# Kernel optimization log

Measured on AMD Instinct MI355X. Metric: run time of the kernel, lower is better.

Reference implementation:

```python
import jax, jax.numpy as jnp
import numpy as np

B, C, H, W = 128, 512, 14, 14
P = 512  # num_parts (codebook size)


def setup_inputs() -> dict:
    key = jax.random.key(0)
    k1, k2, k3 = jax.random.split(key, 3)
    fm = jax.random.normal(k1, (B, C, H, W), dtype=jnp.float32)
    embedding = jax.random.normal(k2, (B, C), dtype=jnp.float32)
    # self.w = torch.randn(P, C).clamp_(min=0)
    w = jnp.maximum(jax.random.normal(k3, (P, C), dtype=jnp.float32), 0.0)
    w_ep_sum = w  # clone of w at init
    w_ep_num = jnp.ones((P,), dtype=jnp.float32)
    return {"fm": fm, "embedding": embedding, "w": w,
            "w_ep_sum": w_ep_sum, "w_ep_num": w_ep_num, "epoch": 5}


def reference(fm, embedding, w, w_ep_sum, w_ep_num, epoch):
    b, c, h, wd = fm.shape
    p = w.shape[0]
    # NCHW -> [B, HW, C]
    x = jnp.transpose(fm, (0, 2, 3, 1)).reshape(b, h * wd, c)
    xf = x.reshape(b * h * wd, c)
    dist = (jnp.sum(xf * xf, axis=1, keepdims=True)
            + jnp.sum(w * w, axis=1)
            - 2.0 * (xf @ w.T))                      # [B*HW, P]
    assign = jax.nn.softmax(-dist.reshape(b, h * wd, p), axis=-1)
    # hard threshold: zero out weak assignments
    assign = jnp.where(assign < 1.0 / p, 0.0, assign)  # [B, HW, P]
    assign_sum = assign.mean(axis=1)                    # [B, P]

    if epoch > 2:  # epoch is a static Python int
        # relu(einsum('bn,nc->bnc').mean(1)) == relu((assign_sum @ w) / P)
        cvec = jax.nn.relu((assign_sum @ w) / p)        # [B, C]
        embedding_cat = jnp.concatenate([embedding, cvec], axis=-1)
    else:
        embedding_cat = jnp.concatenate([embedding, jnp.zeros_like(embedding)], axis=-1)

    # collect_weight (no-grad EMA-style accumulate).
    # einsum('bmn,bmc->bmnc').sum(1).sum(0) == einsum('bmn,bmc->nc') -- avoids
    # materializing the [B,M,N,C] tensor the torch code builds.
    update_w = jnp.einsum('bmn,bmc->nc', assign, x)     # [P, C]
    assign_mean = jnp.sum(assign, axis=(0, 1))          # [P]
    upd = assign_mean > 1.0
    new_w_ep_sum = jnp.where(upd[:, None], w_ep_sum + update_w, w_ep_sum)
    new_w_ep_num = jnp.where(upd, w_ep_num + assign_mean, w_ep_num)
    return embedding_cat, new_w_ep_sum, new_w_ep_num
```

## Files before the change

### kernel.cpp

```cpp
#include <hip/hip_runtime.h>
#include <hip/hip_bf16.h>

#define Bn   128
#define Cn   512
#define HWn  196
#define Mn   25088
#define Pn   512
#define SPLITK2 32
#define KCH  1024

#define OFF_XT     0u
#define OFF_AT     8388608u
#define OFF_PART   16777216u
#define OFF_XM     16777216u
#define OFF_WF     25165824u
#define OFF_WNORM  25296896u
#define OFF_RAWP   25297408u
#define OFF_MEAN   25559552u

#define OUT_CAT  0u
#define OUT_WSUM 131072u
#define OUT_WNUM 393216u

using bf16x8 = __attribute__((ext_vector_type(8))) short;
using f16x8  = __attribute__((ext_vector_type(8))) _Float16;
using f32x4  = __attribute__((ext_vector_type(4))) float;

__device__ __forceinline__ unsigned short f2b(float f) {
    union { float f; unsigned u; } x; x.f = f;
    unsigned r = x.u + 0x7fffu + ((x.u >> 16) & 1u);
    return (unsigned short)(r >> 16);
}

__global__ __launch_bounds__(64) void k_wnorm(const float* __restrict__ w,
                                              float* __restrict__ wn,
                                              _Float16* __restrict__ wf) {
    int n = blockIdx.x, l = threadIdx.x;
    const float* p = w + (size_t)n * Cn + l * 8;
    float4 a = *(const float4*)p;
    float4 b = *(const float4*)(p + 4);
    float s = a.x*a.x + a.y*a.y + a.z*a.z + a.w*a.w
            + b.x*b.x + b.y*b.y + b.z*b.z + b.w*b.w;
    alignas(16) _Float16 h[8];
    h[0]=(_Float16)a.x; h[1]=(_Float16)a.y; h[2]=(_Float16)a.z; h[3]=(_Float16)a.w;
    h[4]=(_Float16)b.x; h[5]=(_Float16)b.y; h[6]=(_Float16)b.z; h[7]=(_Float16)b.w;
    *(float4*)(wf + (size_t)(n >> 4) * 8192u + (size_t)(l >> 2) * 512
                 + (n & 15) * 32 + (l & 3) * 8) = *(const float4*)h;
    #pragma unroll
    for (int o = 32; o > 0; o >>= 1) s += __shfl_down(s, o);
    if (l == 0) wn[n] = s;
}

__global__ __launch_bounds__(512) void k_prep2(const float* __restrict__ fm,
                                               _Float16* __restrict__ xm,
                                               unsigned short* __restrict__ xt) {
    __shared__ _Float16 tile[64][200];
    int b = blockIdx.x;
    int cg = blockIdx.y * 64;
    int t = threadIdx.x;
    for (int i = t; i < 64 * 49; i += 512) {
        int cl = i / 49, h4 = i - cl * 49;
        float4 v = *(const float4*)(fm + ((size_t)(b * Cn + cg + cl) * HWn) + h4 * 4);
        tile[cl][h4*4+0] = (_Float16)v.x;
        tile[cl][h4*4+1] = (_Float16)v.y;
        tile[cl][h4*4+2] = (_Float16)v.z;
        tile[cl][h4*4+3] = (_Float16)v.w;
    }
    __syncthreads();
    for (int i = t; i < HWn * 8; i += 512) {
        int hw = i >> 3, seg = i & 7;
        alignas(16) _Float16 h[8];
        #pragma unroll
        for (int j = 0; j < 8; ++j) h[j] = tile[seg * 8 + j][hw];
        *(float4*)(xm + (size_t)(b * HWn + hw) * Cn + cg + seg * 8) = *(const float4*)h;
    }
    for (int i = t; i < 64 * 4 * 16; i += 512) {
        int cl = i >> 6, rem = i & 63;
        int q = rem >> 4, j4 = rem & 15;
        ushort4 o;
        if (j4 < 12) {
            o.x = f2b((float)tile[cl][q*49 + j4*4 + 0]);
            o.y = f2b((float)tile[cl][q*49 + j4*4 + 1]);
            o.z = f2b((float)tile[cl][q*49 + j4*4 + 2]);
            o.w = f2b((float)tile[cl][q*49 + j4*4 + 3]);
        } else if (j4 == 12) {
            o.x = f2b((float)tile[cl][q*49 + 48]);
            o.y = 0; o.z = 0; o.w = 0;
        } else {
            o.x = 0; o.y = 0; o.z = 0; o.w = 0;
        }
        int c = cg + cl;
        int T = c >> 4;
        int seg = b * 8 + q * 2 + (j4 >> 3);
        int k = (j4 & 7) * 4;
        *(ushort4*)(xt + (size_t)T * 524288u + (size_t)seg * 512 + (c & 15) * 32 + k) = o;
    }
}

__global__ __launch_bounds__(512, 2) void k_post(const _Float16* __restrict__ xm,
                                                 const _Float16* __restrict__ wf,
                                                 const float* __restrict__ wnorm,
                                                 unsigned short* __restrict__ at,
                                                 float* __restrict__ rawp) {
    __shared__ _Float16 As[64][72];
    __shared__ float redmx[64][8];
    __shared__ float redsm[64][8];
    const int bid = blockIdx.x;
    const int b = bid >> 2, q = bid & 3;
    const int tid = threadIdx.x;
    const int nq = tid >> 6, lane = tid & 63;
    const int rl = lane & 15, rq = lane >> 4;
    const int kb = rq * 8;
    const int m0 = b * 196 + q * 49;
    const int n0 = nq * 64;
    const int srow = tid >> 3;
    const int skc  = tid & 7;
    const bool sOK = srow < 49;
    const _Float16* asrc = xm + (size_t)(m0 + srow) * Cn + skc * 8;

    if (!sOK) {
        f16x8 z = {};
        *(f16x8*)&As[srow][skc * 8] = z;
    }
    if (sOK) *(f16x8*)&As[srow][skc * 8] = *(const f16x8*)asrc;
    __syncthreads();

    const _Float16* wtb = wf + (size_t)(nq * 4) * 8192u + rl * 32 + kb;

    f32x4 acc[4][4] = {};
    for (int c = 0; c < 8; ++c) {
        #pragma unroll
        for (int ks = 0; ks < 2; ++ks) {
            const int seg = c * 2 + ks;
            f16x8 a[4], bb[4];
            #pragma unroll
            for (int f = 0; f < 4; ++f)
                a[f] = *(const f16x8*)&As[f * 16 + rl][ks * 32 + kb];
            #pragma unroll
            for (int g = 0; g < 4; ++g)
                bb[g] = *(const f16x8*)(wtb + (size_t)g * 8192u + seg * 512);
            #pragma unroll
            for (int f = 0; f < 4; ++f)
                #pragma unroll
                for (int g = 0; g < 4; ++g)
                    acc[f][g] = __builtin_amdgcn_mfma_f32_16x16x32_f16(a[f], bb[g], acc[f][g], 0, 0, 0);
        }
        if (c < 7) {
            __syncthreads();
            if (sOK)
                *(f16x8*)&As[srow][skc * 8] = *(const f16x8*)(asrc + (c + 1) * 64);
            __syncthreads();
        }
    }
    float wn4[4];
    #pragma unroll
    for (int g = 0; g < 4; ++g) wn4[g] = wnorm[n0 + g * 16 + rl];
    #pragma unroll
    for (int f = 0; f < 4; ++f)
        #pragma unroll
        for (int g = 0; g < 4; ++g)
            #pragma unroll
            for (int r = 0; r < 4; ++r)
                acc[f][g][r] = 2.0f * acc[f][g][r] - wn4[g];
    float mx[4][4];
    #pragma unroll
    for (int f = 0; f < 4; ++f)
        #pragma unroll
        for (int r = 0; r < 4; ++r) {
            float m_ = fmaxf(fmaxf(acc[f][0][r], acc[f][1][r]),
                             fmaxf(acc[f][2][r], acc[f][3][r]));
            #pragma unroll
            for (int o = 8; o >= 1; o >>= 1) m_ = fmaxf(m_, __shfl_xor(m_, o));
            mx[f][r] = m_;
        }
    if (rl == 0)
        #pragma unroll
        for (int f = 0; f < 4; ++f)
            #pragma unroll
            for (int r = 0; r < 4; ++r)
                redmx[f * 16 + rq * 4 + r][nq] = mx[f][r];
    __syncthreads();
    float rmax[4][4];
    #pragma unroll
    for (int f = 0; f < 4; ++f)
        #pragma unroll
        for (int r = 0; r < 4; ++r) {
            const float* p = redmx[f * 16 + rq * 4 + r];
            rmax[f][r] = fmaxf(fmaxf(fmaxf(p[0], p[1]), fmaxf(p[2], p[3])),
                               fmaxf(fmaxf(p[4], p[5]), fmaxf(p[6], p[7])));
        }
    float sm[4][4];
    #pragma unroll
    for (int f = 0; f < 4; ++f)
        #pragma unroll
        for (int r = 0; r < 4; ++r) {
            float s_ = 0.f;
            #pragma unroll
            for (int g = 0; g < 4; ++g) {
                float p = __expf(acc[f][g][r] - rmax[f][r]);
                acc[f][g][r] = p;
                s_ += p;
            }
            #pragma unroll
            for (int o = 8; o >= 1; o >>= 1) s_ += __shfl_xor(s_, o);
            sm[f][r] = s_;
        }
    if (rl == 0)
        #pragma unroll
        for (int f = 0; f < 4; ++f)
            #pragma unroll
            for (int r = 0; r < 4; ++r)
                redsm[f * 16 + rq * 4 + r][nq] = sm[f][r];
    __syncthreads();
    const float invP = 1.0f / 512.0f;
    #pragma unroll
    for (int f = 0; f < 4; ++f)
        #pragma unroll
        for (int r = 0; r < 4; ++r) {
            const float* p = redsm[f * 16 + rq * 4 + r];
            float inv = 1.0f / (p[0] + p[1] + p[2] + p[3] + p[4] + p[5] + p[6] + p[7]);
            #pragma unroll
            for (int g = 0; g < 4; ++g) {
                float a = acc[f][g][r] * inv;
                acc[f][g][r] = (a < invP) ? 0.0f : a;
            }
        }
    float cs[4] = {};
    #pragma unroll
    for (int g = 0; g < 4; ++g) {
        #pragma unroll
        for (int f = 0; f < 4; ++f)
            #pragma unroll
            for (int r = 0; r < 4; ++r)
                if (f * 16 + rq * 4 + r < 49) cs[g] += acc[f][g][r];
        cs[g] += __shfl_xor(cs[g], 16);
        cs[g] += __shfl_xor(cs[g], 32);
    }
    if (rq == 0)
        #pragma unroll
        for (int g = 0; g < 4; ++g)
            rawp[(size_t)bid * 512 + n0 + g * 16 + rl] = cs[g];
    const int segbase = b * 8 + q * 2;
    #pragma unroll
    for (int f = 0; f < 4; ++f) {
        const int mloc = f * 16 + rq * 4;
        const int sa = segbase + (mloc >> 5);
        const int k = mloc & 31;
        #pragma unroll
        for (int g = 0; g < 4; ++g) {
            ushort4 o;
            o.x = (mloc + 0 < 49) ? f2b(acc[f][g][0]) : (unsigned short)0;
            o.y = (mloc + 1 < 49) ? f2b(acc[f][g][1]) : (unsigned short)0;
            o.z = (mloc + 2 < 49) ? f2b(acc[f][g][2]) : (unsigned short)0;
            o.w = (mloc + 3 < 49) ? f2b(acc[f][g][3]) : (unsigned short)0;
            const int T = nq * 4 + g;
            *(ushort4*)(at + (size_t)T * 524288u + (size_t)sa * 512 + rl * 32 + k) = o;
        }
    }
}

__global__ __launch_bounds__(256) void k_reduce(const float* __restrict__ rawp,
                                                const float* __restrict__ wnum,
                                                float* __restrict__ mean,
                                                float* __restrict__ outnum) {
    int n = blockIdx.x * 256 + threadIdx.x;
    float s = 0.f;
    for (int r = 0; r < 512; ++r) s += rawp[(size_t)r * Pn + n];
    mean[n] = s;
    outnum[n] = wnum[n] + (s > 1.0f ? s : 0.0f);
}

__global__ __launch_bounds__(256) void k_cvec(const float* __restrict__ rawp,
                                              const float* __restrict__ w,
                                              const float* __restrict__ emb,
                                              const int* __restrict__ epoch,
                                              float* __restrict__ out) {
    __shared__ float srow[512];
    int b = blockIdx.x, t = threadIdx.x;
    float s0 = 0.f, s1 = 0.f;
    #pragma unroll
    for (int q = 0; q < 4; ++q) {
        s0 += rawp[(size_t)(4 * b + q) * Pn + t];
        s1 += rawp[(size_t)(4 * b + q) * Pn + t + 256];
    }
    srow[t] = s0;
    srow[t + 256] = s1;
    __syncthreads();
    float a0 = 0.f, a1 = 0.f;
    for (int p = 0; p < Pn; ++p) {
        float ap = srow[p];
        a0 = fmaf(ap, w[(size_t)p * Cn + t], a0);
        a1 = fmaf(ap, w[(size_t)p * Cn + t + 256], a1);
    }
    const float sc = 1.0f / (196.0f * 512.0f);
    int ep = epoch[0];
    float c0 = (ep > 2) ? fmaxf(a0, 0.f) * sc : 0.f;
    float c1 = (ep > 2) ? fmaxf(a1, 0.f) * sc : 0.f;
    out[(size_t)b * 1024 + t]             = emb[(size_t)b * Cn + t];
    out[(size_t)b * 1024 + t + 256]       = emb[(size_t)b * Cn + t + 256];
    out[(size_t)b * 1024 + 512 + t]       = c0;
    out[(size_t)b * 1024 + 512 + t + 256] = c1;
}

__global__ __launch_bounds__(256) void k_upw_mfma(const unsigned short* __restrict__ at,
                                                  const unsigned short* __restrict__ xt,
                                                  float* __restrict__ part) {
    const int id = blockIdx.x;
    const int sp = id & 31;
    const int m  = id >> 5;
    const int tid = threadIdx.x;
    const int wave = tid >> 6, lane = tid & 63;
    const int wn = wave >> 1, wc = wave & 1;
    const int n0 = (m & 3) * 128;
    const int c0 = (m >> 2) * 128;
    const int rl = lane & 15, rq = lane >> 4;
    const int loff = rl * 32 + rq * 8;
    const int segbase = sp * 32;

    const unsigned short* pa[4];
    const unsigned short* pb[4];
    #pragma unroll
    for (int f = 0; f < 4; ++f) {
        const int Ta = (n0 >> 4) + wn * 4 + f;
        const int Tb = (c0 >> 4) + wc * 4 + f;
        pa[f] = at + (size_t)Ta * 524288u + (size_t)segbase * 512 + loff;
        pb[f] = xt + (size_t)Tb * 524288u + (size_t)segbase * 512 + loff;
    }

    f32x4 acc[4][4] = {};
    bf16x8 aC[4], bC[4], aN[4], bN[4];
    #pragma unroll
    for (int f = 0; f < 4; ++f) {
        aC[f] = *(const bf16x8*)(pa[f]);
        bC[f] = *(const bf16x8*)(pb[f]);
    }
    for (int ks = 0; ks < 32; ks += 2) {
        #pragma unroll
        for (int f = 0; f < 4; ++f) {
            aN[f] = *(const bf16x8*)(pa[f] + (ks + 1) * 512);
            bN[f] = *(const bf16x8*)(pb[f] + (ks + 1) * 512);
        }
        #pragma unroll
        for (int i = 0; i < 4; ++i)
            #pragma unroll
            for (int j = 0; j < 4; ++j)
                acc[i][j] = __builtin_amdgcn_mfma_f32_16x16x32_bf16(aC[i], bC[j], acc[i][j], 0, 0, 0);
        if (ks + 2 < 32) {
            #pragma unroll
            for (int f = 0; f < 4; ++f) {
                aC[f] = *(const bf16x8*)(pa[f] + (ks + 2) * 512);
                bC[f] = *(const bf16x8*)(pb[f] + (ks + 2) * 512);
            }
        }
        #pragma unroll
        for (int i = 0; i < 4; ++i)
            #pragma unroll
            for (int j = 0; j < 4; ++j)
                acc[i][j] = __builtin_amdgcn_mfma_f32_16x16x32_bf16(aN[i], bN[j], acc[i][j], 0, 0, 0);
    }
    float* o = part + (size_t)sp * (Pn * Cn);
    const int rq4 = rq * 4;
    #pragma unroll
    for (int i = 0; i < 4; ++i) {
        #pragma unroll
        for (int j = 0; j < 4; ++j) {
            int n = n0 + wn * 64 + i * 16 + rq4;
            int c = c0 + wc * 64 + j * 16 + rl;
            #pragma unroll
            for (int r = 0; r < 4; ++r)
                o[(size_t)(n + r) * Cn + c] = acc[i][j][r];
        }
    }
}

__global__ __launch_bounds__(256) void k_wep(const float* __restrict__ part,
                                             const float* __restrict__ mean,
                                             const float* __restrict__ wsum,
                                             float* __restrict__ out1) {
    int n = blockIdx.x, t = threadIdx.x;
    bool upd = mean[n] > 1.0f;
    #pragma unroll
    for (int cc = 0; cc < 2; ++cc) {
        int c = t + cc * 256;
        float s = 0.f;
        #pragma unroll
        for (int k = 0; k < SPLITK2; ++k)
            s += part[(size_t)k * (Pn * Cn) + (size_t)n * Cn + c];
        size_t idx = (size_t)n * Cn + c;
        out1[idx] = wsum[idx] + (upd ? s : 0.f);
    }
}

extern "C" void kernel_launch(void* const* d_in, const int* in_sizes, int n_in,
                              void* d_out, int out_size, void* d_ws, size_t ws_size,
                              hipStream_t stream) {
    const float* fm    = (const float*)d_in[0];
    const float* emb   = (const float*)d_in[1];
    const float* w     = (const float*)d_in[2];
    const float* wsum  = (const float*)d_in[3];
    const float* wnum  = (const float*)d_in[4];
    const int*   epoch = (const int*)d_in[5];
    float* out = (float*)d_out;
    float* wsf = (float*)d_ws;

    unsigned short* xtb   = (unsigned short*)(wsf + OFF_XT);
    unsigned short* atb   = (unsigned short*)(wsf + OFF_AT);
    float*          partb = wsf + OFF_PART;
    _Float16*       xmb   = (_Float16*)(wsf + OFF_XM);
    _Float16*       wfb   = (_Float16*)(wsf + OFF_WF);
    float*          wnormb = wsf + OFF_WNORM;
    float*          rawpb  = wsf + OFF_RAWP;
    float*          meanb  = wsf + OFF_MEAN;

    k_wnorm<<<512, 64, 0, stream>>>(w, wnormb, wfb);
    k_prep2<<<dim3(Bn, 8), 512, 0, stream>>>(fm, xmb, xtb);
    k_post<<<512, 512, 0, stream>>>(xmb, wfb, wnormb, atb, rawpb);
    k_reduce<<<2, 256, 0, stream>>>(rawpb, wnum, meanb, out + OUT_WNUM);
    k_cvec<<<Bn, 256, 0, stream>>>(rawpb, w, emb, epoch, out + OUT_CAT);
    k_upw_mfma<<<512, 256, 0, stream>>>(atb, xtb, partb);
    k_wep<<<Pn, 256, 0, stream>>>(partb, meanb, wsum, out + OUT_WSUM);
}
```

Baseline: 170.9 us.

## Double split-K with bf16 partials and stage full A tile in LDS

The update-weight GEMM split-K doubles from 32 to 64 and launches 1024 blocks, so more blocks are in flight. Partial sums are stored as bf16 instead of fp32, which keeps the workspace size the same and halves the bytes per partial that k_wep reads, at the cost of precision in the accumulated update. k_post now loads the whole 64x512 activation tile into LDS once, removing the per-chunk reload and its barriers, and raises the launch-bounds occupancy hint to 4. The larger LDS footprint (about 70KB per block) may cap how many blocks fit on a CU regardless of that hint.

Result: faster. 161.9 us (-5.3%).

```diff
diff --git a/kernel.cpp b/kernel.cpp
--- a/kernel.cpp
+++ b/kernel.cpp
@@ -6,8 +6,8 @@
 #define HWn  196
 #define Mn   25088
 #define Pn   512
-#define SPLITK2 32
-#define KCH  1024
+#define SPLITK2 64
+#define KCH  512
 
 #define OFF_XT     0u
 #define OFF_AT     8388608u
@@ -30,6 +30,10 @@
     union { float f; unsigned u; } x; x.f = f;
     unsigned r = x.u + 0x7fffu + ((x.u >> 16) & 1u);
     return (unsigned short)(r >> 16);
+}
+__device__ __forceinline__ float b2f(unsigned short u) {
+    union { unsigned u; float f; } x; x.u = ((unsigned)u) << 16;
+    return x.f;
 }
 
 __global__ __launch_bounds__(64) void k_wnorm(const float* __restrict__ w,
@@ -97,12 +101,12 @@
     }
 }
 
-__global__ __launch_bounds__(512, 2) void k_post(const _Float16* __restrict__ xm,
+__global__ __launch_bounds__(512, 4) void k_post(const _Float16* __restrict__ xm,
                                                  const _Float16* __restrict__ wf,
                                                  const float* __restrict__ wnorm,
                                                  unsigned short* __restrict__ at,
                                                  float* __restrict__ rawp) {
-    __shared__ _Float16 As[64][72];
+    __shared__ _Float16 As[64][520];
     __shared__ float redmx[64][8];
     __shared__ float redsm[64][8];
     const int bid = blockIdx.x;
@@ -113,44 +117,34 @@
     const int kb = rq * 8;
     const int m0 = b * 196 + q * 49;
     const int n0 = nq * 64;
-    const int srow = tid >> 3;
-    const int skc  = tid & 7;
-    const bool sOK = srow < 49;
-    const _Float16* asrc = xm + (size_t)(m0 + srow) * Cn + skc * 8;
-
-    if (!sOK) {
-        f16x8 z = {};
-        *(f16x8*)&As[srow][skc * 8] = z;
-    }
-    if (sOK) *(f16x8*)&As[srow][skc * 8] = *(const f16x8*)asrc;
+
+    for (int i = tid; i < 64 * 64; i += 512) {
+        int row = i >> 6, kc = (i & 63) * 8;
+        if (row < 49)
+            *(f16x8*)&As[row][kc] = *(const f16x8*)(xm + (size_t)(m0 + row) * Cn + kc);
+        else {
+            f16x8 z = {};
+            *(f16x8*)&As[row][kc] = z;
+        }
+    }
     __syncthreads();
 
     const _Float16* wtb = wf + (size_t)(nq * 4) * 8192u + rl * 32 + kb;
 
     f32x4 acc[4][4] = {};
-    for (int c = 0; c < 8; ++c) {
-        #pragma unroll
-        for (int ks = 0; ks < 2; ++ks) {
-            const int seg = c * 2 + ks;
-            f16x8 a[4], bb[4];
-            #pragma unroll
-            for (int f = 0; f < 4; ++f)
-                a[f] = *(const f16x8*)&As[f * 16 + rl][ks * 32 + kb];
+    for (int seg = 0; seg < 16; ++seg) {
+        f16x8 a[4], bb[4];
+        #pragma unroll
+        for (int f = 0; f < 4; ++f)
+            a[f] = *(const f16x8*)&As[f * 16 + rl][seg * 32 + kb];
+        #pragma unroll
+        for (int g = 0; g < 4; ++g)
+            bb[g] = *(const f16x8*)(wtb + (size_t)g * 8192u + seg * 512);
+        #pragma unroll
+        for (int f = 0; f < 4; ++f)
             #pragma unroll
             for (int g = 0; g < 4; ++g)
-                bb[g] = *(const f16x8*)(wtb + (size_t)g * 8192u + seg * 512);
-            #pragma unroll
-            for (int f = 0; f < 4; ++f)
-                #pragma unroll
-                for (int g = 0; g < 4; ++g)
-                    acc[f][g] = __builtin_amdgcn_mfma_f32_16x16x32_f16(a[f], bb[g], acc[f][g], 0, 0, 0);
-        }
-        if (c < 7) {
-            __syncthreads();
-            if (sOK)
-                *(f16x8*)&As[srow][skc * 8] = *(const f16x8*)(asrc + (c + 1) * 64);
-            __syncthreads();
-        }
+                acc[f][g] = __builtin_amdgcn_mfma_f32_16x16x32_f16(a[f], bb[g], acc[f][g], 0, 0, 0);
     }
     float wn4[4];
     #pragma unroll
@@ -304,10 +298,10 @@
 
 __global__ __launch_bounds__(256) void k_upw_mfma(const unsigned short* __restrict__ at,
                                                   const unsigned short* __restrict__ xt,
-                                                  float* __restrict__ part) {
+                                                  unsigned short* __restrict__ part) {
     const int id = blockIdx.x;
-    const int sp = id & 31;
-    const int m  = id >> 5;
+    const int sp = id & 63;
+    const int m  = id >> 6;
     const int tid = threadIdx.x;
     const int wave = tid >> 6, lane = tid & 63;
     const int wn = wave >> 1, wc = wave & 1;
@@ -315,7 +309,7 @@
     const int c0 = (m >> 2) * 128;
     const int rl = lane & 15, rq = lane >> 4;
     const int loff = rl * 32 + rq * 8;
-    const int segbase = sp * 32;
+    const int segbase = sp * 16;
 
     const unsigned short* pa[4];
     const unsigned short* pb[4];
@@ -334,7 +328,7 @@
         aC[f] = *(const bf16x8*)(pa[f]);
         bC[f] = *(const bf16x8*)(pb[f]);
     }
-    for (int ks = 0; ks < 32; ks += 2) {
+    for (int ks = 0; ks < 16; ks += 2) {
         #pragma unroll
         for (int f = 0; f < 4; ++f) {
             aN[f] = *(const bf16x8*)(pa[f] + (ks + 1) * 512);
@@ -345,7 +339,7 @@
             #pragma unroll
             for (int j = 0; j < 4; ++j)
                 acc[i][j] = __builtin_amdgcn_mfma_f32_16x16x32_bf16(aC[i], bC[j], acc[i][j], 0, 0, 0);
-        if (ks + 2 < 32) {
+        if (ks + 2 < 16) {
             #pragma unroll
             for (int f = 0; f < 4; ++f) {
                 aC[f] = *(const bf16x8*)(pa[f] + (ks + 2) * 512);
@@ -358,7 +352,7 @@
             for (int j = 0; j < 4; ++j)
                 acc[i][j] = __builtin_amdgcn_mfma_f32_16x16x32_bf16(aN[i], bN[j], acc[i][j], 0, 0, 0);
     }
-    float* o = part + (size_t)sp * (Pn * Cn);
+    unsigned short* o = part + (size_t)sp * (Pn * Cn);
     const int rq4 = rq * 4;
     #pragma unroll
     for (int i = 0; i < 4; ++i) {
@@ -368,12 +362,12 @@
             int c = c0 + wc * 64 + j * 16 + rl;
             #pragma unroll
             for (int r = 0; r < 4; ++r)
-                o[(size_t)(n + r) * Cn + c] = acc[i][j][r];
-        }
-    }
-}
-
-__global__ __launch_bounds__(256) void k_wep(const float* __restrict__ part,
+                o[(size_t)(n + r) * Cn + c] = f2b(acc[i][j][r]);
+        }
+    }
+}
+
+__global__ __launch_bounds__(256) void k_wep(const unsigned short* __restrict__ part,
                                              const float* __restrict__ mean,
                                              const float* __restrict__ wsum,
                                              float* __restrict__ out1) {
@@ -385,7 +379,7 @@
         float s = 0.f;
         #pragma unroll
         for (int k = 0; k < SPLITK2; ++k)
-            s += part[(size_t)k * (Pn * Cn) + (size_t)n * Cn + c];
+            s += b2f(part[(size_t)k * (Pn * Cn) + (size_t)n * Cn + c]);
         size_t idx = (size_t)n * Cn + c;
         out1[idx] = wsum[idx] + (upd ? s : 0.f);
     }
@@ -405,7 +399,7 @@
 
     unsigned short* xtb   = (unsigned short*)(wsf + OFF_XT);
     unsigned short* atb   = (unsigned short*)(wsf + OFF_AT);
-    float*          partb = wsf + OFF_PART;
+    unsigned short* partb = (unsigned short*)(wsf + OFF_PART);
     _Float16*       xmb   = (_Float16*)(wsf + OFF_XM);
     _Float16*       wfb   = (_Float16*)(wsf + OFF_WF);
     float*          wnormb = wsf + OFF_WNORM;
@@ -417,6 +411,6 @@
     k_post<<<512, 512, 0, stream>>>(xmb, wfb, wnormb, atb, rawpb);
     k_reduce<<<2, 256, 0, stream>>>(rawpb, wnum, meanb, out + OUT_WNUM);
     k_cvec<<<Bn, 256, 0, stream>>>(rawpb, w, emb, epoch, out + OUT_CAT);
-    k_upw_mfma<<<512, 256, 0, stream>>>(atb, xtb, partb);
+    k_upw_mfma<<<1024, 256, 0, stream>>>(atb, xtb, partb);
     k_wep<<<Pn, 256, 0, stream>>>(partb, meanb, wsum, out + OUT_WSUM);
 }
```
